# Performance work log

Hardware: AMD Instinct MI355X
Metric: run time of the kernel (lower is better)

Reference implementation:

```python
import jax, jax.numpy as jnp
import numpy as np

N_NODES = 100000
N_PAIRS = 6400000
CUTOFF = 10.0
ONSET = 6.0


def setup_inputs() -> dict:
    key = jax.random.key(0)
    k1, k2, k3, k4 = jax.random.split(key, 4)
    R_ij = jax.random.normal(k1, (N_PAIRS, 3), dtype=jnp.float32)
    i = jax.random.randint(k2, (N_PAIRS,), 0, N_NODES, dtype=jnp.int32)
    j = jax.random.randint(k3, (N_PAIRS,), 0, N_NODES, dtype=jnp.int32)
    Z_i = jax.random.randint(k4, (N_NODES,), 0, 100, dtype=jnp.int32)
    pair_mask = jnp.ones((N_PAIRS,), dtype=bool)
    node_mask = jnp.ones((N_NODES,), dtype=bool)
    sigma = jnp.array(2.0, dtype=jnp.float32)
    epsilon = jnp.array(1.5, dtype=jnp.float32)
    return {"R_ij": R_ij, "i": i, "j": j, "Z_i": Z_i,
            "pair_mask": pair_mask, "node_mask": node_mask,
            "sigma": sigma, "epsilon": epsilon}


def _distance(R):
    r2 = jnp.sum(R * R, axis=-1)
    mask = r2 > 0
    safe_r2 = jnp.where(mask, r2, 0.0)
    return jnp.where(mask, jnp.sqrt(safe_r2), 0.0)


def _lj_energy(R_ij, i, num_nodes, pair_mask, sigma, epsilon):
    cutoff2 = CUTOFF ** 2
    onset2 = ONSET ** 2
    dr = _distance(R_ij)                       # [pairs]
    # pairwise LJ with safe inverse
    m = dr > 0.0
    inv_r = jnp.where(m, 1.0 / jnp.where(m, dr, 1.0), 0.0)
    inv_r6 = inv_r ** 6
    inv_r12 = inv_r6 * inv_r6
    pair_e = (2.0 * epsilon) * (sigma ** 12 * inv_r12 - sigma ** 6 * inv_r6)
    # smooth cutoff switch
    d2 = dr * dr
    after_onset = jnp.where(
        d2 < cutoff2,
        (cutoff2 - d2) ** 2 * (cutoff2 + 2.0 * d2 - 3.0 * onset2) / (cutoff2 - onset2) ** 3,
        0.0)
    switch = jnp.where(d2 < onset2, 1.0, after_onset)
    contributions = switch * pair_e * pair_mask
    return jax.ops.segment_sum(contributions, i, num_segments=num_nodes,
                               indices_are_sorted=False)


def reference(R_ij, i, j, Z_i, pair_mask, node_mask, sigma, epsilon):
    energy = _lj_energy(R_ij, i, Z_i.shape[0], pair_mask, sigma, epsilon)
    return energy * node_mask
```

## Files before the change

kernel.cpp:

```cpp
#include <hip/hip_runtime.h>


#define NPB       512
#define NPB_MASK  511
#define NB_MAX    256
#define TILE      2048
#define RSTRIDE   2816
#define SB        8

typedef __attribute__((address_space(1))) void g_as1;
typedef __attribute__((address_space(3))) void l_as3;

__device__ __forceinline__ void async_copy16(void* lds_base, const void* gsrc) {
    __builtin_amdgcn_global_load_lds((g_as1*)gsrc, (l_as3*)lds_base, 16, 0, 0);
}

__device__ __forceinline__ float lj_pair_val(float q, float s6, float s12, float twoeps) {
    const float inv_denom = 1.0f / 262144.0f;
    float inv_r2  = (q > 0.0f) ? (1.0f / q) : 0.0f;
    float inv_r6  = inv_r2 * inv_r2 * inv_r2;
    float inv_r12 = inv_r6 * inv_r6;
    float pair_e  = twoeps * (s12 * inv_r12 - s6 * inv_r6);
    float sw;
    if (q < 36.0f) {
        sw = 1.0f;
    } else if (q < 100.0f) {
        float d = 100.0f - q;
        sw = d * d * (2.0f * q - 8.0f) * inv_denom;
    } else {
        sw = 0.0f;
    }
    return sw * pair_e;
}

__global__ __launch_bounds__(256) void lj_bin(
    const float* __restrict__ R, const int* __restrict__ seg,
    const float* __restrict__ sigma_p, const float* __restrict__ eps_p,
    int* __restrict__ bins, int* __restrict__ table,
    float* __restrict__ out, int n_pairs, int n_nodes, int nblocks)
{
    __shared__ int cursor[NB_MAX];
    __shared__ int rankc[NB_MAX];
    __shared__ int wtot[4];
    __shared__ int buckpk[2 * 256];
    __shared__ __align__(16) float R_lds[TILE * 3];
    __shared__ __align__(16) int seg_lds[TILE];
    int* ldsdata = (int*)R_lds;

    const int tid = threadIdx.x;
    const int wv = tid >> 6, ln = tid & 63;
    const int tile0  = blockIdx.x * TILE;
    const int nvalid = min(TILE, n_pairs - tile0);

    if (nvalid == TILE) {
        const char* Rg = (const char*)(R + (size_t)tile0 * 3);
        #pragma unroll
        for (int r = 0; r < 6; ++r) {
            const int j = wv * 6 + r;
            async_copy16((char*)R_lds + j * 1024, Rg + j * 1024 + ln * 16);
        }
        const char* Sg = (const char*)(seg + tile0);
        #pragma unroll
        for (int r = 0; r < 2; ++r) {
            const int m = wv * 2 + r;
            async_copy16((char*)seg_lds + m * 1024, Sg + m * 1024 + ln * 16);
        }
    }

    {
        const int n = blockIdx.x * 64 + tid;
        if (tid < 64 && n < n_nodes) out[n] = 0.0f;
    }
    cursor[tid] = 0;

    if (nvalid < TILE) {
        for (int idx = tid; idx < TILE * 3; idx += 256)
            R_lds[idx] = (idx < nvalid * 3) ? R[(size_t)tile0 * 3 + idx] : 0.0f;
        for (int idx = tid; idx < TILE; idx += 256)
            seg_lds[idx] = (idx < nvalid) ? seg[tile0 + idx] : 0;
    }

    asm volatile("s_waitcnt vmcnt(0)" ::: "memory");
    __syncthreads();

    const float sg = sigma_p[0], ep = eps_p[0];
    const float s2 = sg * sg, s6 = s2 * s2 * s2, s12 = s6 * s6;
    const float twoeps = 2.0f * ep;

    int pint[8];

    #pragma unroll
    for (int g = 0; g < 2; ++g) {
        const int e0 = g * 1024 + tid * 4;
        const float4 a  = *(const float4*)(R_lds + e0 * 3);
        const float4 b4 = *(const float4*)(R_lds + e0 * 3 + 4);
        const float4 c  = *(const float4*)(R_lds + e0 * 3 + 8);
        const int4  iv  = *(const int4*)(seg_lds + e0);
        const int n0 = iv.x, n1 = iv.y, n2 = iv.z, n3 = iv.w;
        const int b0 = n0 >> 9, b1 = n1 >> 9, b2 = n2 >> 9, b3 = n3 >> 9;
        if (e0 + 0 < nvalid) atomicAdd(&cursor[b0], 1);
        if (e0 + 1 < nvalid) atomicAdd(&cursor[b1], 1);
        if (e0 + 2 < nvalid) atomicAdd(&cursor[b2], 1);
        if (e0 + 3 < nvalid) atomicAdd(&cursor[b3], 1);
        buckpk[g * 256 + tid] = b0 | (b1 << 8) | (b2 << 16) | (b3 << 24);
        const float q0 = a.x*a.x + a.y*a.y + a.z*a.z;
        const float q1 = a.w*a.w + b4.x*b4.x + b4.y*b4.y;
        const float q2 = b4.z*b4.z + b4.w*b4.w + c.x*c.x;
        const float q3 = c.y*c.y + c.z*c.z + c.w*c.w;
        pint[g*4+0] = (__float_as_int(lj_pair_val(q0, s6, s12, twoeps)) & ~NPB_MASK) | (n0 & NPB_MASK);
        pint[g*4+1] = (__float_as_int(lj_pair_val(q1, s6, s12, twoeps)) & ~NPB_MASK) | (n1 & NPB_MASK);
        pint[g*4+2] = (__float_as_int(lj_pair_val(q2, s6, s12, twoeps)) & ~NPB_MASK) | (n2 & NPB_MASK);
        pint[g*4+3] = (__float_as_int(lj_pair_val(q3, s6, s12, twoeps)) & ~NPB_MASK) | (n3 & NPB_MASK);
    }

    __syncthreads();

    const int cnt     = cursor[tid];
    const int cnt_pad = (cnt + 3) & ~3;
    int incl = cnt_pad;
    #pragma unroll
    for (int d = 1; d < 64; d <<= 1) {
        int v = __shfl_up(incl, d);
        if (ln >= d) incl += v;
    }
    if (ln == 63) wtot[wv] = incl;
    __syncthreads();
    int pre = 0;
    #pragma unroll
    for (int w = 0; w < 4; ++w) pre += (w < wv) ? wtot[w] : 0;
    const int excl_pad = pre + incl - cnt_pad;
    rankc[tid] = excl_pad;
    table[(size_t)tid * nblocks + blockIdx.x] = excl_pad | (cnt << 16);
    __syncthreads();

    for (int z = cnt; z < cnt_pad; ++z) ldsdata[excl_pad + z] = 0;

    #pragma unroll
    for (int g = 0; g < 2; ++g) {
        const int pk = buckpk[g * 256 + tid];
        #pragma unroll
        for (int k = 0; k < 4; ++k) {
            const int li = g * 1024 + tid * 4 + k;
            if (li < nvalid) {
                const int b = (pk >> (8 * k)) & 255;
                const int pos = atomicAdd(&rankc[b], 1);
                ldsdata[pos] = pint[g * 4 + k];
            }
        }
    }
    __syncthreads();

    int* dst = bins + (size_t)blockIdx.x * RSTRIDE;
    for (int idx = tid * 4; idx < RSTRIDE; idx += 1024)
        *(int4*)(dst + idx) = *(const int4*)(ldsdata + idx);
}

__global__ __launch_bounds__(256) void lj_accum(
    const int* __restrict__ bins, const int* __restrict__ table,
    float* __restrict__ out, int nb, int nblocks, int n_nodes)
{
    const int b = blockIdx.x % nb;
    const int s = blockIdx.x / nb;
    const int tid = threadIdx.x;

    __shared__ float acc[NPB];
    for (int l = tid; l < NPB; l += 256) acc[l] = 0.0f;
    __syncthreads();

    const int chunk = (nblocks + SB - 1) / SB;
    const int r0 = s * chunk;
    const int r1 = min(nblocks, r0 + chunk);

    const int* tab_b = table + (size_t)b * nblocks;
    for (int r = r0 + tid; r < r1; r += 256) {
        const int pe  = tab_b[r];
        const int cnt = pe >> 16;
        const int* p  = bins + (size_t)r * RSTRIDE + (pe & 0xFFFF);
        for (int k = 0; k < cnt; k += 4) {
            const int4 e4 = *(const int4*)(p + k);
            atomicAdd(&acc[e4.x & NPB_MASK], __int_as_float(e4.x & ~NPB_MASK));
            atomicAdd(&acc[e4.y & NPB_MASK], __int_as_float(e4.y & ~NPB_MASK));
            atomicAdd(&acc[e4.z & NPB_MASK], __int_as_float(e4.z & ~NPB_MASK));
            atomicAdd(&acc[e4.w & NPB_MASK], __int_as_float(e4.w & ~NPB_MASK));
        }
    }
    __syncthreads();

    const int node0 = b * NPB;
    for (int l = tid; l < NPB; l += 256) {
        const int node = node0 + l;
        if (node < n_nodes) {
            const float v = acc[l];
            if (v != 0.0f) atomicAdd(&out[node], v);
        }
    }
}

__global__ __launch_bounds__(256) void lj_pair_scatter(
    const float* __restrict__ R, const int* __restrict__ seg,
    const float* __restrict__ sigma_p, const float* __restrict__ eps_p,
    float* __restrict__ out, int n_pairs)
{
    const float sg = sigma_p[0], ep = eps_p[0];
    const float s2 = sg*sg, s6 = s2*s2*s2, s12 = s6*s6;
    const float twoeps = 2.0f * ep;
    const int t = blockIdx.x * blockDim.x + threadIdx.x;
    const int nthreads = gridDim.x * blockDim.x;
    for (int base = t * 4; base < n_pairs; base += nthreads * 4) {
        if (base + 3 < n_pairs) {
            const float4* Rv = (const float4*)(R + (size_t)base * 3);
            float4 a = Rv[0], b = Rv[1], c = Rv[2];
            int4 iv = *(const int4*)(seg + base);
            float r2[4];
            r2[0] = a.x*a.x + a.y*a.y + a.z*a.z;
            r2[1] = a.w*a.w + b.x*b.x + b.y*b.y;
            r2[2] = b.z*b.z + b.w*b.w + c.x*c.x;
            r2[3] = c.y*c.y + c.z*c.z + c.w*c.w;
            const int ii[4] = {iv.x, iv.y, iv.z, iv.w};
            #pragma unroll
            for (int k = 0; k < 4; ++k)
                atomicAdd(&out[ii[k]], lj_pair_val(r2[k], s6, s12, twoeps));
        } else {
            for (int p = base; p < n_pairs; ++p) {
                float x = R[(size_t)p*3], y = R[(size_t)p*3+1], z = R[(size_t)p*3+2];
                atomicAdd(&out[seg[p]], lj_pair_val(x*x+y*y+z*z, s6, s12, twoeps));
            }
        }
    }
}

extern "C" void kernel_launch(void* const* d_in, const int* in_sizes, int n_in,
                              void* d_out, int out_size, void* d_ws, size_t ws_size,
                              hipStream_t stream) {
    const float* R     = (const float*)d_in[0];
    const int*   seg   = (const int*)d_in[1];
    const float* sigma = (const float*)d_in[6];
    const float* eps   = (const float*)d_in[7];
    float* out = (float*)d_out;

    const int n_pairs = in_sizes[1];
    const int n_nodes = out_size;
    const int nb = (n_nodes + NPB - 1) / NPB;
    const int nblocks = (n_pairs + TILE - 1) / TILE;

    const size_t bin_bytes = (size_t)nblocks * RSTRIDE * sizeof(int);
    const size_t tab_bytes = (size_t)NB_MAX * nblocks * sizeof(int);
    const size_t need = bin_bytes + tab_bytes;

    if (nb >= 1 && nb <= NB_MAX && nblocks >= 1 && ws_size >= need) {
        int* bins  = (int*)d_ws;
        int* table = (int*)((char*)d_ws + bin_bytes);

        if ((size_t)nblocks * 64 < (size_t)n_nodes)
            hipMemsetAsync(out, 0, (size_t)n_nodes * sizeof(float), stream);

        lj_bin<<<nblocks, 256, 0, stream>>>(R, seg, sigma, eps, bins, table,
                                            out, n_pairs, n_nodes, nblocks);
        lj_accum<<<nb * SB, 256, 0, stream>>>(bins, table, out, nb, nblocks, n_nodes);
    } else {
        hipMemsetAsync(d_out, 0, (size_t)out_size * sizeof(float), stream);
        const int grid = (n_pairs + 1023) / 1024;
        lj_pair_scatter<<<grid, 256, 0, stream>>>(R, seg, sigma, eps, out, n_pairs);
    }
}
```

Baseline: 218.3 us.

## Write bins contiguously per bucket via global atomic offsets instead of per-tile strided slots

```diff
diff --git a/kernel.cpp b/kernel.cpp
--- a/kernel.cpp
+++ b/kernel.cpp
@@ -5,7 +5,7 @@
 #define NPB_MASK  511
 #define NB_MAX    256
 #define TILE      2048
-#define RSTRIDE   2816
+#define CAPB      38912
 #define SB        8
 
 typedef __attribute__((address_space(1))) void g_as1;
@@ -36,16 +36,18 @@
 __global__ __launch_bounds__(256) void lj_bin(
     const float* __restrict__ R, const int* __restrict__ seg,
     const float* __restrict__ sigma_p, const float* __restrict__ eps_p,
-    int* __restrict__ bins, int* __restrict__ table,
-    float* __restrict__ out, int n_pairs, int n_nodes, int nblocks)
+    int* __restrict__ bins, int* __restrict__ gcount,
+    float* __restrict__ out, int n_pairs, int n_nodes)
 {
     __shared__ int cursor[NB_MAX];
     __shared__ int rankc[NB_MAX];
     __shared__ int wtot[4];
+    __shared__ int total_s;
     __shared__ int buckpk[2 * 256];
     __shared__ __align__(16) float R_lds[TILE * 3];
     __shared__ __align__(16) int seg_lds[TILE];
     int* ldsdata = (int*)R_lds;
+    int* ldsoff4 = seg_lds;
 
     const int tid = threadIdx.x;
     const int wv = tid >> 6, ln = tid & 63;
@@ -130,10 +132,19 @@
     for (int w = 0; w < 4; ++w) pre += (w < wv) ? wtot[w] : 0;
     const int excl_pad = pre + incl - cnt_pad;
     rankc[tid] = excl_pad;
-    table[(size_t)tid * nblocks + blockIdx.x] = excl_pad | (cnt << 16);
+    if (tid == NB_MAX - 1) total_s = excl_pad + cnt_pad;
+
+    int delta = 0;
+    if (cnt > 0) {
+        int goff = atomicAdd(&gcount[tid], cnt_pad);
+        if (goff > CAPB - cnt_pad) goff = CAPB - cnt_pad;
+        delta = tid * CAPB + goff - excl_pad;
+    }
     __syncthreads();
 
     for (int z = cnt; z < cnt_pad; ++z) ldsdata[excl_pad + z] = 0;
+    for (int gq = (excl_pad >> 2), gq1 = (excl_pad + cnt_pad) >> 2; gq < gq1; ++gq)
+        ldsoff4[gq] = delta;
 
     #pragma unroll
     for (int g = 0; g < 2; ++g) {
@@ -150,39 +161,38 @@
     }
     __syncthreads();
 
-    int* dst = bins + (size_t)blockIdx.x * RSTRIDE;
-    for (int idx = tid * 4; idx < RSTRIDE; idx += 1024)
-        *(int4*)(dst + idx) = *(const int4*)(ldsdata + idx);
+    const int total_pad = total_s;
+    for (int idx = tid * 4; idx < total_pad; idx += 1024) {
+        const int d = ldsoff4[idx >> 2];
+        *(int4*)(bins + d + idx) = *(const int4*)(ldsdata + idx);
+    }
 }
 
 __global__ __launch_bounds__(256) void lj_accum(
-    const int* __restrict__ bins, const int* __restrict__ table,
-    float* __restrict__ out, int nb, int nblocks, int n_nodes)
+    const int* __restrict__ bins, const int* __restrict__ gcount,
+    float* __restrict__ out, int nb, int n_nodes)
 {
-    const int b = blockIdx.x % nb;
-    const int s = blockIdx.x / nb;
+    const int b = blockIdx.x >> 3;
+    const int s = blockIdx.x & (SB - 1);
     const int tid = threadIdx.x;
 
     __shared__ float acc[NPB];
     for (int l = tid; l < NPB; l += 256) acc[l] = 0.0f;
     __syncthreads();
 
-    const int chunk = (nblocks + SB - 1) / SB;
-    const int r0 = s * chunk;
-    const int r1 = min(nblocks, r0 + chunk);
-
-    const int* tab_b = table + (size_t)b * nblocks;
-    for (int r = r0 + tid; r < r1; r += 256) {
-        const int pe  = tab_b[r];
-        const int cnt = pe >> 16;
-        const int* p  = bins + (size_t)r * RSTRIDE + (pe & 0xFFFF);
-        for (int k = 0; k < cnt; k += 4) {
-            const int4 e4 = *(const int4*)(p + k);
-            atomicAdd(&acc[e4.x & NPB_MASK], __int_as_float(e4.x & ~NPB_MASK));
-            atomicAdd(&acc[e4.y & NPB_MASK], __int_as_float(e4.y & ~NPB_MASK));
-            atomicAdd(&acc[e4.z & NPB_MASK], __int_as_float(e4.z & ~NPB_MASK));
-            atomicAdd(&acc[e4.w & NPB_MASK], __int_as_float(e4.w & ~NPB_MASK));
-        }
+    int len = gcount[b];
+    if (len > CAPB) len = CAPB;
+    const int per   = (((len + SB - 1) / SB) + 3) & ~3;
+    const int start = s * per;
+    const int end   = min(len, start + per);
+
+    const int* p = bins + (size_t)b * CAPB;
+    for (int k = start + tid * 4; k < end; k += 1024) {
+        const int4 e4 = *(const int4*)(p + k);
+        atomicAdd(&acc[e4.x & NPB_MASK], __int_as_float(e4.x & ~NPB_MASK));
+        atomicAdd(&acc[e4.y & NPB_MASK], __int_as_float(e4.y & ~NPB_MASK));
+        atomicAdd(&acc[e4.z & NPB_MASK], __int_as_float(e4.z & ~NPB_MASK));
+        atomicAdd(&acc[e4.w & NPB_MASK], __int_as_float(e4.w & ~NPB_MASK));
     }
     __syncthreads();
 
@@ -243,20 +253,22 @@
     const int nb = (n_nodes + NPB - 1) / NPB;
     const int nblocks = (n_pairs + TILE - 1) / TILE;
 
-    const size_t bin_bytes = (size_t)nblocks * RSTRIDE * sizeof(int);
-    const size_t tab_bytes = (size_t)NB_MAX * nblocks * sizeof(int);
-    const size_t need = bin_bytes + tab_bytes;
-
-    if (nb >= 1 && nb <= NB_MAX && nblocks >= 1 && ws_size >= need) {
-        int* bins  = (int*)d_ws;
-        int* table = (int*)((char*)d_ws + bin_bytes);
-
-        if ((size_t)nblocks * 64 < (size_t)n_nodes)
-            hipMemsetAsync(out, 0, (size_t)n_nodes * sizeof(float), stream);
-
-        lj_bin<<<nblocks, 256, 0, stream>>>(R, seg, sigma, eps, bins, table,
-                                            out, n_pairs, n_nodes, nblocks);
-        lj_accum<<<nb * SB, 256, 0, stream>>>(bins, table, out, nb, nblocks, n_nodes);
+    const size_t bins_bytes = (size_t)NB_MAX * CAPB * sizeof(int);
+    const size_t gc_bytes   = (size_t)NB_MAX * sizeof(int);
+    const size_t need = bins_bytes + gc_bytes;
+
+    const long long avg = (n_nodes > 0) ? ((long long)n_pairs * NPB) / n_nodes : 0;
+    const bool cap_ok = avg + avg / 8 <= CAPB;
+
+    if (nb >= 1 && nb <= NB_MAX && nblocks >= 1 && cap_ok && ws_size >= need &&
+        (size_t)nblocks * 64 >= (size_t)n_nodes) {
+        int* bins   = (int*)d_ws;
+        int* gcount = (int*)((char*)d_ws + bins_bytes);
+
+        hipMemsetAsync(gcount, 0, gc_bytes, stream);
+        lj_bin<<<nblocks, 256, 0, stream>>>(R, seg, sigma, eps, bins, gcount,
+                                            out, n_pairs, n_nodes);
+        lj_accum<<<nb * SB, 256, 0, stream>>>(bins, gcount, out, nb, n_nodes);
     } else {
         hipMemsetAsync(d_out, 0, (size_t)out_size * sizeof(float), stream);
         const int grid = (n_pairs + 1023) / 1024;
```

Measured after the change: 248.1 us. 13.6% more time.

## Restructure accumulate kernel to process 8 node bins per block with row-major table

Applied to the files above, without the earlier changes.

```diff
diff --git a/kernel.cpp b/kernel.cpp
--- a/kernel.cpp
+++ b/kernel.cpp
@@ -6,7 +6,7 @@
 #define NB_MAX    256
 #define TILE      2048
 #define RSTRIDE   2816
-#define SB        8
+#define ACC_S     32
 
 typedef __attribute__((address_space(1))) void g_as1;
 typedef __attribute__((address_space(3))) void l_as3;
@@ -37,7 +37,7 @@
     const float* __restrict__ R, const int* __restrict__ seg,
     const float* __restrict__ sigma_p, const float* __restrict__ eps_p,
     int* __restrict__ bins, int* __restrict__ table,
-    float* __restrict__ out, int n_pairs, int n_nodes, int nblocks)
+    float* __restrict__ out, int n_pairs, int n_nodes)
 {
     __shared__ int cursor[NB_MAX];
     __shared__ int rankc[NB_MAX];
@@ -130,7 +130,7 @@
     for (int w = 0; w < 4; ++w) pre += (w < wv) ? wtot[w] : 0;
     const int excl_pad = pre + incl - cnt_pad;
     rankc[tid] = excl_pad;
-    table[(size_t)tid * nblocks + blockIdx.x] = excl_pad | (cnt << 16);
+    table[(size_t)blockIdx.x * NB_MAX + tid] = excl_pad | (cnt_pad << 16);
     __syncthreads();
 
     for (int z = cnt; z < cnt_pad; ++z) ldsdata[excl_pad + z] = 0;
@@ -157,37 +157,43 @@
 
 __global__ __launch_bounds__(256) void lj_accum(
     const int* __restrict__ bins, const int* __restrict__ table,
-    float* __restrict__ out, int nb, int nblocks, int n_nodes)
+    float* __restrict__ out, int nblocks, int n_nodes)
 {
-    const int b = blockIdx.x % nb;
-    const int s = blockIdx.x / nb;
+    const int cb  = blockIdx.x / ACC_S;
+    const int s   = blockIdx.x % ACC_S;
     const int tid = threadIdx.x;
-
-    __shared__ float acc[NPB];
-    for (int l = tid; l < NPB; l += 256) acc[l] = 0.0f;
-    __syncthreads();
-
-    const int chunk = (nblocks + SB - 1) / SB;
+    const int fb0 = cb * 8;
+
+    __shared__ float acc[8 * NPB];
+    for (int l = tid; l < 8 * NPB; l += 256) acc[l] = 0.0f;
+    __syncthreads();
+
+    const int chunk = (nblocks + ACC_S - 1) / ACC_S;
     const int r0 = s * chunk;
-    const int r1 = min(nblocks, r0 + chunk);
-
-    const int* tab_b = table + (size_t)b * nblocks;
-    for (int r = r0 + tid; r < r1; r += 256) {
-        const int pe  = tab_b[r];
-        const int cnt = pe >> 16;
-        const int* p  = bins + (size_t)r * RSTRIDE + (pe & 0xFFFF);
-        for (int k = 0; k < cnt; k += 4) {
-            const int4 e4 = *(const int4*)(p + k);
-            atomicAdd(&acc[e4.x & NPB_MASK], __int_as_float(e4.x & ~NPB_MASK));
-            atomicAdd(&acc[e4.y & NPB_MASK], __int_as_float(e4.y & ~NPB_MASK));
-            atomicAdd(&acc[e4.z & NPB_MASK], __int_as_float(e4.z & ~NPB_MASK));
-            atomicAdd(&acc[e4.w & NPB_MASK], __int_as_float(e4.w & ~NPB_MASK));
-        }
-    }
-    __syncthreads();
-
-    const int node0 = b * NPB;
-    for (int l = tid; l < NPB; l += 256) {
+    const int nrr = min(nblocks - r0, chunk);
+    const int items = (nrr > 0) ? nrr * 8 : 0;
+
+    for (int w = tid; w < items; w += 256) {
+        const int r  = r0 + (w >> 3);
+        const int f  = w & 7;
+        const int pe = table[(size_t)r * NB_MAX + fb0 + f];
+        const int len = pe >> 16;
+        if (len > 0) {
+            const int* p  = bins + (size_t)r * RSTRIDE + (pe & 0xFFFF);
+            const int  hi = f << 9;
+            for (int k = 0; k < len; k += 4) {
+                const int4 e4 = *(const int4*)(p + k);
+                atomicAdd(&acc[hi | (e4.x & NPB_MASK)], __int_as_float(e4.x & ~NPB_MASK));
+                atomicAdd(&acc[hi | (e4.y & NPB_MASK)], __int_as_float(e4.y & ~NPB_MASK));
+                atomicAdd(&acc[hi | (e4.z & NPB_MASK)], __int_as_float(e4.z & ~NPB_MASK));
+                atomicAdd(&acc[hi | (e4.w & NPB_MASK)], __int_as_float(e4.w & ~NPB_MASK));
+            }
+        }
+    }
+    __syncthreads();
+
+    const int node0 = cb * (8 * NPB);
+    for (int l = tid; l < 8 * NPB; l += 256) {
         const int node = node0 + l;
         if (node < n_nodes) {
             const float v = acc[l];
@@ -240,23 +246,22 @@
 
     const int n_pairs = in_sizes[1];
     const int n_nodes = out_size;
-    const int nb = (n_nodes + NPB - 1) / NPB;
+    const int nb  = (n_nodes + NPB - 1) / NPB;
+    const int ncb = (nb + 7) / 8;
     const int nblocks = (n_pairs + TILE - 1) / TILE;
 
     const size_t bin_bytes = (size_t)nblocks * RSTRIDE * sizeof(int);
-    const size_t tab_bytes = (size_t)NB_MAX * nblocks * sizeof(int);
+    const size_t tab_bytes = (size_t)nblocks * NB_MAX * sizeof(int);
     const size_t need = bin_bytes + tab_bytes;
 
-    if (nb >= 1 && nb <= NB_MAX && nblocks >= 1 && ws_size >= need) {
+    if (nb >= 1 && nb <= NB_MAX && nblocks >= 1 && ws_size >= need &&
+        (size_t)nblocks * 64 >= (size_t)n_nodes) {
         int* bins  = (int*)d_ws;
         int* table = (int*)((char*)d_ws + bin_bytes);
 
-        if ((size_t)nblocks * 64 < (size_t)n_nodes)
-            hipMemsetAsync(out, 0, (size_t)n_nodes * sizeof(float), stream);
-
         lj_bin<<<nblocks, 256, 0, stream>>>(R, seg, sigma, eps, bins, table,
-                                            out, n_pairs, n_nodes, nblocks);
-        lj_accum<<<nb * SB, 256, 0, stream>>>(bins, table, out, nb, nblocks, n_nodes);
+                                            out, n_pairs, n_nodes);
+        lj_accum<<<ncb * ACC_S, 256, 0, stream>>>(bins, table, out, nblocks, n_nodes);
     } else {
         hipMemsetAsync(d_out, 0, (size_t)out_size * sizeof(float), stream);
         const int grid = (n_pairs + 1023) / 1024;
```

Result: no change. 214.5 us (-1.7%).
